# Kernel tuning notes

Hardware: AMD Instinct MI355X
Metric: run time of the kernel (lower is better)

## Reference

```python
import jax, jax.numpy as jnp
import numpy as np

N, E, G = 50000, 300000, 256
H, LAT, VOCAB = 256, 64, 100
BN_EPS = 1e-5


def _bn(x, gamma, beta):
    # BatchNorm1d in training mode: per-feature batch mean / biased var
    mu = x.mean(axis=0)
    var = x.var(axis=0)
    return gamma * (x - mu) * jax.lax.rsqrt(var + BN_EPS) + beta


def _gconv(x, edge_attr, src, dst):
    # message: softplus(x_j + e), aggregate: scatter-add to dst, update: +(1+eps)*x with eps=0
    m = jax.nn.softplus(x[src] + edge_attr)          # [E, H]
    agg = jax.ops.segment_sum(m, dst, num_segments=N)  # [N, H]
    return agg + x


def setup_inputs() -> dict:
    key = jax.random.key(0)
    ks = jax.random.split(key, 16)
    inp = {
        "node_type": jax.random.randint(ks[0], (N,), 0, VOCAB),
        "edge_type": jax.random.randint(ks[1], (E,), 0, VOCAB),
        "edge_index": jax.random.randint(ks[2], (2, E), 0, N),
        "batch": jnp.sort(jax.random.randint(ks[3], (N,), 0, G)),
        "node_emb_w": jax.random.normal(ks[4], (VOCAB, H), jnp.float32),
        "edge_emb_w": jax.random.normal(ks[5], (VOCAB, H), jnp.float32),
        "g1": jnp.ones((H,), jnp.float32), "b1": jnp.zeros((H,), jnp.float32),
        "g2": jnp.ones((H,), jnp.float32), "b2": jnp.zeros((H,), jnp.float32),
        "g3": jnp.ones((H,), jnp.float32), "b3": jnp.zeros((H,), jnp.float32),
        "go1": jnp.ones((H,), jnp.float32), "bo1": jnp.zeros((H,), jnp.float32),
        "go2": jnp.ones((H // 2,), jnp.float32), "bo2": jnp.zeros((H // 2,), jnp.float32),
        "W1": jax.random.normal(ks[6], (2 * H, H), jnp.float32) * (2 * H) ** -0.5,
        "B1": jnp.zeros((H,), jnp.float32),
        "W2": jax.random.normal(ks[7], (H, H // 2), jnp.float32) * H ** -0.5,
        "B2": jnp.zeros((H // 2,), jnp.float32),
        "W3": jax.random.normal(ks[8], (H // 2, 2 * LAT), jnp.float32) * (H // 2) ** -0.5,
        "B3": jnp.zeros((2 * LAT,), jnp.float32),
    }
    return inp


def reference(node_type, edge_type, edge_index, batch,
              node_emb_w, edge_emb_w,
              g1, b1, g2, b2, g3, b3, go1, bo1, go2, bo2,
              W1, B1, W2, B2, W3, B3):
    act = jax.nn.softplus
    src, dst = edge_index[0], edge_index[1]
    h = node_emb_w[node_type]            # [N, H]
    e = edge_emb_w[edge_type]            # [E, H]
    h = act(_bn(_gconv(h, e, src, dst), g1, b1))
    h = act(_bn(_gconv(h, e, src, dst), g2, b2))
    h = _bn(_gconv(h, e, src, dst), g3, b3)
    h_global = jax.ops.segment_sum(h, batch, num_segments=G)  # [G, H]
    feat = jnp.concatenate([h, h_global[batch]], axis=-1)     # [N, 2H]
    feat = act(_bn(feat @ W1 + B1, go1, bo1))
    feat = act(_bn(feat @ W2 + B2, go2, bo2))
    out = feat @ W3 + B3                                      # [N, 2*LAT]
    return out[:, :LAT], out[:, LAT:]
```

## Files before the change

kernel.cpp:

```cpp
#include <hip/hip_runtime.h>
#include <hip/hip_bf16.h>

namespace {

constexpr int N = 50000;
constexpr int E = 300000;
constexpr int G = 256;
constexpr int H = 256;
constexpr float EPS = 1e-5f;
constexpr int NB = (N + 255) / 256;
constexpr int POOL_S = 16;
constexpr int GBL = 256;
constexpr int NVB = N / 16;
constexpr float LOG2E = 1.4426950408889634f;
constexpr float LN2   = 0.6931471805599453f;

typedef unsigned short u16;
typedef __attribute__((ext_vector_type(8))) short bf16x8;
typedef __attribute__((ext_vector_type(4))) float f32x4;

__device__ __forceinline__ float expnabs(float z){
  float r; asm("v_exp_f32 %0, -abs(%1)" : "=v"(r) : "v"(z)); return r;
}
__device__ __forceinline__ float log2f_(float x){
  float r; asm("v_log_f32 %0, %1" : "=v"(r) : "v"(x)); return r;
}
__device__ __forceinline__ float spw(float zs){
  return fmaxf(zs, 0.f) + log2f_(1.f + expnabs(zs));
}
__device__ __forceinline__ u16 f2b(float f){
  union { float f; unsigned u; } v; v.f = f;
  unsigned r = v.u + 0x7FFF + ((v.u >> 16) & 1);
  return (u16)(r >> 16);
}
__device__ __forceinline__ float b2f(u16 u){
  union { unsigned i; float f; } v; v.i = ((unsigned)u) << 16; return v.f;
}
__device__ __forceinline__ float4 b2f4(ushort4 u){
  return make_float4(b2f(u.x), b2f(u.y), b2f(u.z), b2f(u.w));
}
__device__ __forceinline__ ushort4 f2b4(float4 v){
  ushort4 o; o.x = f2b(v.x); o.y = f2b(v.y); o.z = f2b(v.z); o.w = f2b(v.w);
  return o;
}

__device__ __forceinline__ void gl_lds16(const u16* g, u16* l){
  __builtin_amdgcn_global_load_lds(
      (const __attribute__((address_space(1))) unsigned int*)g,
      (__attribute__((address_space(3))) unsigned int*)l, 16, 0, 0);
}

__global__ void k_pre(const int* __restrict__ nt, const float* __restrict__ nemb,
                      u16* __restrict__ xb, const int* __restrict__ dst,
                      int* __restrict__ cnt,
                      const float* __restrict__ W1, const float* __restrict__ W2,
                      const float* __restrict__ W3, const float* __restrict__ eemb,
                      u16* __restrict__ Wt1, u16* __restrict__ Wt2,
                      u16* __restrict__ Wt3, float* __restrict__ eembF){
  int idx = blockIdx.x * 256 + threadIdx.x;
  if (idx < N * 64){
    int i = idx >> 6, fq = (idx & 63) << 2;
    float4 v = *(const float4*)(nemb + (size_t)nt[i] * H + fq);
    v.x *= LOG2E; v.y *= LOG2E; v.z *= LOG2E; v.w *= LOG2E;
    *(ushort4*)(xb + (size_t)i * H + fq) = f2b4(v);
    return;
  }
  int j = idx - N * 64;
  if (j < E){ atomicAdd(&cnt[dst[j]], 1); return; }
  j -= E;
  if (j < 65536){ int c = j >> 8, k = j & 255; Wt1[j] = f2b(W1[(size_t)k * 256 + c]); return; }
  j -= 65536;
  if (j < 32768){ int c = j >> 8, k = j & 255; Wt2[j] = f2b(W2[(size_t)k * 128 + c]); return; }
  j -= 32768;
  if (j < 16384){ int c = j >> 7, k = j & 127; Wt3[j] = f2b(W3[(size_t)k * 128 + c]); return; }
  j -= 16384;
  if (j < 25600) eembF[j] = eemb[j] * LOG2E;
}

__global__ void k_scan1(const int* __restrict__ cnt, int* __restrict__ bsum){
  __shared__ int s[256];
  int t = threadIdx.x;
  int i = blockIdx.x * 256 + t;
  s[t] = (i < N) ? cnt[i] : 0;
  __syncthreads();
  for (int d = 128; d > 0; d >>= 1){
    if (t < d) s[t] += s[t + d];
    __syncthreads();
  }
  if (t == 0) bsum[blockIdx.x] = s[0];
}

__global__ void k_scan2(const int* __restrict__ bsum, int* __restrict__ bbase){
  __shared__ int s[256];
  int t = threadIdx.x;
  int orig = (t < NB) ? bsum[t] : 0;
  s[t] = orig;
  __syncthreads();
  for (int d = 1; d < 256; d <<= 1){
    int v = (t >= d) ? s[t - d] : 0;
    __syncthreads();
    s[t] += v;
    __syncthreads();
  }
  bbase[t] = s[t] - orig;
}

__global__ void k_scan3(const int* __restrict__ cnt, const int* __restrict__ bbase,
                        int* __restrict__ off, int* __restrict__ cur){
  __shared__ int s[256];
  int t = threadIdx.x;
  int i = blockIdx.x * 256 + t;
  int v = (i < N) ? cnt[i] : 0;
  s[t] = v;
  __syncthreads();
  for (int d = 1; d < 256; d <<= 1){
    int u = (t >= d) ? s[t - d] : 0;
    __syncthreads();
    s[t] += u;
    __syncthreads();
  }
  int excl = bbase[blockIdx.x] + s[t] - v;
  if (i < N){ off[i] = excl; cur[i] = excl; }
  if (i == N - 1) off[N] = excl + v;
}

__global__ void k_fill(const int* __restrict__ src, const int* __restrict__ dst,
                       const int* __restrict__ et, int* __restrict__ cur,
                       int2* __restrict__ edges_s){
  int e = blockIdx.x * 256 + threadIdx.x;
  if (e >= E) return;
  int d = dst[e];
  int p = atomicAdd(&cur[d], 1);
  edges_s[p] = make_int2(src[e] << 9, et[e] << 10);
}

__device__ __forceinline__ void acc_w(float4& acc, const float4 xs, const float4 es){
  acc.x += spw(xs.x + es.x);
  acc.y += spw(xs.y + es.y);
  acc.z += spw(xs.z + es.z);
  acc.w += spw(xs.w + es.w);
}

__global__ __launch_bounds__(1024)
void k_gather(const u16* __restrict__ xb, u16* __restrict__ agg,
              const int2* __restrict__ edges_s, const int* __restrict__ off,
              const float* __restrict__ eembF,
              float* __restrict__ sums, float* __restrict__ sumsq){
  __shared__ __align__(16) float elds[25600];
  __shared__ float reds[1024][4];
  __shared__ float reds2[1024][4];
  int tid = threadIdx.x;
  int w = tid >> 6, lane = tid & 63;
  int fx = lane << 3, fe = lane << 4;
  const char* xB = (const char*)xb;
  const char* eL = (const char*)elds;

  {
    const float4* s4 = (const float4*)eembF;
    float4* d4 = (float4*)elds;
    for (int t = tid; t < 6400; t += 1024) d4[t] = s4[t];
  }
  __syncthreads();

  float4 ls = make_float4(0.f, 0.f, 0.f, 0.f);
  float4 ls2 = make_float4(0.f, 0.f, 0.f, 0.f);
  for (int vb = blockIdx.x; vb < NVB; vb += GBL){
    int i = vb * 16 + w;
    float4 acc = b2f4(*(const ushort4*)(xB + ((size_t)i << 9) + fx));
    int lo = off[i], hi = off[i + 1];
    int j = lo;
    for (; j + 4 <= hi; j += 4){
      int2 s0 = edges_s[j + 0];
      int2 s1 = edges_s[j + 1];
      int2 s2 = edges_s[j + 2];
      int2 s3 = edges_s[j + 3];
      ushort4 x0 = *(const ushort4*)(xB + s0.x + fx);
      ushort4 x1 = *(const ushort4*)(xB + s1.x + fx);
      ushort4 x2 = *(const ushort4*)(xB + s2.x + fx);
      ushort4 x3 = *(const ushort4*)(xB + s3.x + fx);
      float4 e0 = *(const float4*)(eL + s0.y + fe);
      float4 e1 = *(const float4*)(eL + s1.y + fe);
      float4 e2 = *(const float4*)(eL + s2.y + fe);
      float4 e3 = *(const float4*)(eL + s3.y + fe);
      acc_w(acc, b2f4(x0), e0);
      acc_w(acc, b2f4(x1), e1);
      acc_w(acc, b2f4(x2), e2);
      acc_w(acc, b2f4(x3), e3);
    }
    if (j + 2 <= hi){
      int2 s0 = edges_s[j + 0];
      int2 s1 = edges_s[j + 1];
      ushort4 x0 = *(const ushort4*)(xB + s0.x + fx);
      ushort4 x1 = *(const ushort4*)(xB + s1.x + fx);
      float4 e0 = *(const float4*)(eL + s0.y + fe);
      float4 e1 = *(const float4*)(eL + s1.y + fe);
      acc_w(acc, b2f4(x0), e0);
      acc_w(acc, b2f4(x1), e1);
      j += 2;
    }
    if (j < hi){
      int2 s0 = edges_s[j];
      ushort4 x0 = *(const ushort4*)(xB + s0.x + fx);
      float4 e0 = *(const float4*)(eL + s0.y + fe);
      acc_w(acc, b2f4(x0), e0);
    }
    acc.x *= LN2; acc.y *= LN2; acc.z *= LN2; acc.w *= LN2;
    ls.x += acc.x; ls.y += acc.y; ls.z += acc.z; ls.w += acc.w;
    ls2.x += acc.x * acc.x; ls2.y += acc.y * acc.y;
    ls2.z += acc.z * acc.z; ls2.w += acc.w * acc.w;
    *(ushort4*)((char*)agg + ((size_t)i << 9) + fx) = f2b4(acc);
  }
  reds[tid][0] = ls.x;  reds[tid][1] = ls.y;  reds[tid][2] = ls.z;  reds[tid][3] = ls.w;
  reds2[tid][0] = ls2.x; reds2[tid][1] = ls2.y; reds2[tid][2] = ls2.z; reds2[tid][3] = ls2.w;
  __syncthreads();
  if (tid < 256){
    int f = tid;
    float ts = 0.f, ts2 = 0.f;
    #pragma unroll
    for (int w2 = 0; w2 < 16; ++w2){
      int s = w2 * 64 + (f >> 2);
      ts += reds[s][f & 3];
      ts2 += reds2[s][f & 3];
    }
    atomicAdd(&sums[f], ts);
    atomicAdd(&sumsq[f], ts2);
  }
}

template<int ACT, int SCALED>
__global__ void k_norm(const u16* __restrict__ in, u16* __restrict__ outb,
                       const float* __restrict__ sums, const float* __restrict__ sumsq,
                       const float* __restrict__ gamma, const float* __restrict__ beta,
                       int n4, int fmask){
  int idx = blockIdx.x * 256 + threadIdx.x;
  if (idx >= n4) return;
  int base = idx << 2;
  int f = base & fmask;
  float4 s = *(const float4*)(sums + f);
  float4 q = *(const float4*)(sumsq + f);
  float4 g = *(const float4*)(gamma + f);
  float4 bt = *(const float4*)(beta + f);
  float4 v = b2f4(*(const ushort4*)(in + base));
  const float inv = 1.f / N;
  float m, var, a, c;
  m = s.x * inv; var = q.x * inv - m * m; a = g.x * rsqrtf(var + EPS); c = bt.x - m * a; v.x = a * v.x + c;
  m = s.y * inv; var = q.y * inv - m * m; a = g.y * rsqrtf(var + EPS); c = bt.y - m * a; v.y = a * v.y + c;
  m = s.z * inv; var = q.z * inv - m * m; a = g.z * rsqrtf(var + EPS); c = bt.z - m * a; v.z = a * v.z + c;
  m = s.w * inv; var = q.w * inv - m * m; a = g.w * rsqrtf(var + EPS); c = bt.w - m * a; v.w = a * v.w + c;
  if (ACT){
    v.x = spw(v.x * LOG2E); v.y = spw(v.y * LOG2E);
    v.z = spw(v.z * LOG2E); v.w = spw(v.w * LOG2E);
    if (!SCALED){ v.x *= LN2; v.y *= LN2; v.z *= LN2; v.w *= LN2; }
  }
  *(ushort4*)(outb + base) = f2b4(v);
}

__global__ void k_pool_seg(const u16* __restrict__ xb, const int* __restrict__ batch,
                           float* __restrict__ hg){
  int g = blockIdx.x, sl = blockIdx.y;
  int f = threadIdx.x;
  int lo = 0, hi = N;
  while (lo < hi){ int m = (lo + hi) >> 1; if (batch[m] < g) lo = m + 1; else hi = m; }
  int start = lo;
  lo = 0; hi = N;
  while (lo < hi){ int m = (lo + hi) >> 1; if (batch[m] < g + 1) lo = m + 1; else hi = m; }
  int end = lo;
  int len = end - start;
  int a = start + (int)((long)len * sl / POOL_S);
  int b = start + (int)((long)len * (sl + 1) / POOL_S);
  if (a >= b) return;
  float s = 0.f;
  for (int i = a; i < b; ++i) s += b2f(xb[(size_t)i * H + f]);
  atomicAdd(&hg[g * H + f], s);
}

__global__ void k_hgw(const float* __restrict__ hg, const float* __restrict__ W1,
                      const float* __restrict__ B1, float* __restrict__ hgW){
  int g = blockIdx.x, c = threadIdx.x;
  float acc = B1[c];
  for (int k = 0; k < H; ++k)
    acc += hg[g * H + k] * W1[(size_t)(H + k) * H + c];
  hgW[g * H + c] = acc;
}

template<int K, int NCOUT, int MODE, int STATS>
__global__ __launch_bounds__(256)
void k_mgemm(const u16* __restrict__ Ab, const u16* __restrict__ Wt,
             const float* __restrict__ epi, const int* __restrict__ batch,
             u16* __restrict__ outb, float* __restrict__ outf,
             float* __restrict__ sums, float* __restrict__ sumsq){
  constexpr int T = K / 64;
  __shared__ __align__(16) u16 smem[32768];
  int tid = threadIdx.x;
  int w = tid >> 6, lane = tid & 63;
  int quad = lane >> 4, l15 = lane & 15;
  int wr = w >> 1, wc = w & 1;
  int rowBase = blockIdx.x * 128 + wr * 64;
  int colTile = blockIdx.y * 128;
  const u16* Ag = Ab + (size_t)blockIdx.x * 128 * K;
  const u16* Bg = Wt + (size_t)colTile * K;

  int w6 = tid & 192;
  auto stage = [&](const u16* gbase, u16* lbuf){
    #pragma unroll
    for (int it = 0; it < 4; ++it){
      int p = it * 256 + tid;
      int row = p >> 3, slot = p & 7;
      const u16* g = gbase + (size_t)row * K + ((slot ^ (row & 7)) << 3);
      gl_lds16(g, smem + ((size_t)((lbuf - smem) + (((it * 256 + w6)) << 3))));
    }
  };

  stage(Ag, smem);
  stage(Bg, smem + 16384);

  f32x4 acc[4][4] = {};
  int xb7 = l15 & 7;
  for (int tt = 0; tt < T; ++tt){
    if (tt + 1 < T){
      int nb = (tt + 1) & 1;
      stage(Ag + (tt + 1) * 64, smem + nb * 8192);
      stage(Bg + (tt + 1) * 64, smem + 16384 + nb * 8192);
    }
    __syncthreads();
    const u16* lA = smem + (tt & 1) * 8192;
    const u16* lB = smem + 16384 + (tt & 1) * 8192;
    #pragma unroll
    for (int ks = 0; ks < 2; ++ks){
      int xs = (((ks << 2) | quad) ^ xb7) << 3;
      bf16x8 a[4], b[4];
      #pragma unroll
      for (int t = 0; t < 4; ++t)
        a[t] = *(const bf16x8*)(lA + ((wr * 64 + t * 16 + l15) << 6) + xs);
      #pragma unroll
      for (int u = 0; u < 4; ++u)
        b[u] = *(const bf16x8*)(lB + ((wc * 64 + u * 16 + l15) << 6) + xs);
      #pragma unroll
      for (int t = 0; t < 4; ++t)
        #pragma unroll
        for (int u = 0; u < 4; ++u)
          acc[t][u] = __builtin_amdgcn_mfma_f32_16x16x32_bf16(a[t], b[u], acc[t][u], 0, 0, 0);
    }
    __syncthreads();
  }

  int colBase = colTile + wc * 64;
  float ls[4] = {0.f, 0.f, 0.f, 0.f};
  float ls2[4] = {0.f, 0.f, 0.f, 0.f};
  #pragma unroll
  for (int t = 0; t < 4; ++t){
    #pragma unroll
    for (int r = 0; r < 4; ++r){
      int row = rowBase + t * 16 + quad * 4 + r;
      if (row >= N) continue;
      int g = (MODE == 0) ? batch[row] : 0;
      #pragma unroll
      for (int u = 0; u < 4; ++u){
        int n = colBase + u * 16 + l15;
        float v = acc[t][u][r];
        if (MODE == 0){
          v += epi[(size_t)g * NCOUT + n];
          outb[(size_t)row * NCOUT + n] = f2b(v);
        } else if (MODE == 1){
          v += epi[n];
          outb[(size_t)row * NCOUT + n] = f2b(v);
        } else {
          v += epi[n];
          if (n < 64) outf[(size_t)row * 64 + n] = v;
          else        outf[(size_t)N * 64 + (size_t)row * 64 + (n - 64)] = v;
        }
        if (STATS){ ls[u] += v; ls2[u] += v * v; }
      }
    }
  }
  if (STATS){
    float (*reds)[4]  = (float (*)[4])smem;
    float (*reds2)[4] = (float (*)[4])(smem + 2048);
    #pragma unroll
    for (int u = 0; u < 4; ++u){ reds[tid][u] = ls[u]; reds2[tid][u] = ls2[u]; }
    __syncthreads();
    int f = tid;
    if (f < 128){
      int fl = f & 15, fu = (f >> 4) & 3, fw = f >> 6;
      float ts = 0.f, ts2 = 0.f;
      #pragma unroll
      for (int r2 = 0; r2 < 2; ++r2)
        #pragma unroll
        for (int q = 0; q < 4; ++q){
          int s = (r2 * 2 + fw) * 64 + q * 16 + fl;
          ts += reds[s][fu]; ts2 += reds2[s][fu];
        }
      atomicAdd(&sums[colTile + f], ts);
      atomicAdd(&sumsq[colTile + f], ts2);
    }
  }
}

}

extern "C" void kernel_launch(void* const* d_in, const int* in_sizes, int n_in,
                              void* d_out, int out_size, void* d_ws, size_t ws_size,
                              hipStream_t stream){
  const int* node_type = (const int*)d_in[0];
  const int* edge_type = (const int*)d_in[1];
  const int* src       = (const int*)d_in[2];
  const int* dst       = src + E;
  const int* batch     = (const int*)d_in[3];
  const float* nemb = (const float*)d_in[4];
  const float* eemb = (const float*)d_in[5];
  const float* gs[3] = {(const float*)d_in[6], (const float*)d_in[8], (const float*)d_in[10]};
  const float* bs[3] = {(const float*)d_in[7], (const float*)d_in[9], (const float*)d_in[11]};
  const float* go1 = (const float*)d_in[12]; const float* bo1 = (const float*)d_in[13];
  const float* go2 = (const float*)d_in[14]; const float* bo2 = (const float*)d_in[15];
  const float* W1 = (const float*)d_in[16]; const float* B1 = (const float*)d_in[17];
  const float* W2 = (const float*)d_in[18]; const float* B2 = (const float*)d_in[19];
  const float* W3 = (const float*)d_in[20]; const float* B3 = (const float*)d_in[21];
  float* outf = (float*)d_out;

  char* p = (char*)d_ws;
  int*   cnt    = (int*)p;              p += (size_t)N * 4;
  float* hg     = (float*)p;            p += (size_t)G * H * 4;
  float* statsA = (float*)p;            p += 5 * 512 * 4;
  size_t zeroBytes = (size_t)p - (size_t)d_ws;
  float* hgW    = (float*)p;            p += (size_t)G * H * 4;
  int*   off    = (int*)p;              p += (size_t)(N + 1) * 4;
  int*   cur    = (int*)p;              p += (size_t)N * 4;
  int*   bsum   = (int*)p;              p += 256 * 4;
  int*   bbase  = (int*)p;              p += 256 * 4;
  int2*  edges_s= (int2*)p;             p += (size_t)E * 8;
  u16*   xb     = (u16*)p;              p += (size_t)N * H * 2;
  u16*   agg    = (u16*)p;              p += (size_t)N * H * 2;
  u16*   xf     = (u16*)p;              p += (size_t)N * 128 * 2;
  u16*   Wt1    = (u16*)p;              p += 65536 * 2;
  u16*   Wt2    = (u16*)p;              p += 32768 * 2;
  u16*   Wt3    = (u16*)p;              p += 16384 * 2;
  float* eembF  = (float*)p;            p += 25600 * 4;
  float* sumsL[5], *sumsqL[5];
  for (int k = 0; k < 5; ++k){ sumsL[k] = statsA + k * 512; sumsqL[k] = statsA + k * 512 + 256; }

  hipMemsetAsync(d_ws, 0, zeroBytes, stream);

  const int preItems = N * 64 + E + 65536 + 32768 + 16384 + 25600;
  k_pre<<<(preItems + 255) / 256, 256, 0, stream>>>(
      node_type, nemb, xb, dst, cnt, W1, W2, W3, eemb, Wt1, Wt2, Wt3, eembF);
  k_scan1<<<NB, 256, 0, stream>>>(cnt, bsum);
  k_scan2<<<1, 256, 0, stream>>>(bsum, bbase);
  k_scan3<<<NB, 256, 0, stream>>>(cnt, bbase, off, cur);
  k_fill<<<(E + 255) / 256, 256, 0, stream>>>(src, dst, edge_type, cur, edges_s);

  for (int l = 0; l < 3; ++l){
    k_gather<<<GBL, 1024, 0, stream>>>(xb, agg, edges_s, off, eembF, sumsL[l], sumsqL[l]);
    if (l < 2)
      k_norm<1, 1><<<(N * 64 + 255) / 256, 256, 0, stream>>>(
          agg, xb, sumsL[l], sumsqL[l], gs[l], bs[l], N * 64, 255);
    else
      k_norm<0, 0><<<(N * 64 + 255) / 256, 256, 0, stream>>>(
          agg, xb, sumsL[l], sumsqL[l], gs[l], bs[l], N * 64, 255);
  }

  {
    dim3 pg(G, POOL_S);
    k_pool_seg<<<pg, H, 0, stream>>>(xb, batch, hg);
  }
  k_hgw<<<G, H, 0, stream>>>(hg, W1, B1, hgW);

  const int RB = (N + 127) / 128;

  k_mgemm<256, 256, 0, 1><<<dim3(RB, 2), 256, 0, stream>>>(
      xb, Wt1, hgW, batch, agg, nullptr, sumsL[3], sumsqL[3]);
  k_norm<1, 0><<<(N * 64 + 255) / 256, 256, 0, stream>>>(
      agg, xb, sumsL[3], sumsqL[3], go1, bo1, N * 64, 255);

  k_mgemm<256, 128, 1, 1><<<dim3(RB, 1), 256, 0, stream>>>(
      xb, Wt2, B2, nullptr, xf, nullptr, sumsL[4], sumsqL[4]);
  k_norm<1, 0><<<(N * 32 + 255) / 256, 256, 0, stream>>>(
      xf, xb, sumsL[4], sumsqL[4], go2, bo2, N * 32, 127);

  k_mgemm<128, 128, 2, 0><<<dim3(RB, 1), 256, 0, stream>>>(
      xb, Wt3, B3, nullptr, nullptr, outf, nullptr, nullptr);
}
```

Before: 455.0 us.

## Store edge embedding table in LDS as fp16 and double gather grid

The edge-embedding table kept in LDS by the gather kernel is switched from fp32 to fp16, halving its shared-memory footprint. The large per-thread reduction arrays are replaced by LDS atomics into 256-entry accumulators, and the grid is doubled from 256 to 512 blocks. Together these cut LDS use per block so more 1024-thread blocks can be resident per CU, raising occupancy for the latency-bound gather. The cost is fp16 rounding of the scaled edge embeddings and contention on the LDS atomics.

Result: slower. 498.8 us (+9.6%).

```diff
diff --git a/kernel.cpp b/kernel.cpp
--- a/kernel.cpp
+++ b/kernel.cpp
@@ -1,5 +1,6 @@
 #include <hip/hip_runtime.h>
 #include <hip/hip_bf16.h>
+#include <hip/hip_fp16.h>
 
 namespace {
 
@@ -10,7 +11,7 @@
 constexpr float EPS = 1e-5f;
 constexpr int NB = (N + 255) / 256;
 constexpr int POOL_S = 16;
-constexpr int GBL = 256;
+constexpr int GBL = 512;
 constexpr int NVB = N / 16;
 constexpr float LOG2E = 1.4426950408889634f;
 constexpr float LN2   = 0.6931471805599453f;
@@ -18,6 +19,7 @@
 typedef unsigned short u16;
 typedef __attribute__((ext_vector_type(8))) short bf16x8;
 typedef __attribute__((ext_vector_type(4))) float f32x4;
+typedef _Float16 f16x4 __attribute__((ext_vector_type(4)));
 
 __device__ __forceinline__ float expnabs(float z){
   float r; asm("v_exp_f32 %0, -abs(%1)" : "=v"(r) : "v"(z)); return r;
@@ -56,7 +58,7 @@
                       const float* __restrict__ W1, const float* __restrict__ W2,
                       const float* __restrict__ W3, const float* __restrict__ eemb,
                       u16* __restrict__ Wt1, u16* __restrict__ Wt2,
-                      u16* __restrict__ Wt3, float* __restrict__ eembF){
+                      u16* __restrict__ Wt3, u16* __restrict__ eembH){
   int idx = blockIdx.x * 256 + threadIdx.x;
   if (idx < N * 64){
     int i = idx >> 6, fq = (idx & 63) << 2;
@@ -74,7 +76,10 @@
   j -= 32768;
   if (j < 16384){ int c = j >> 7, k = j & 127; Wt3[j] = f2b(W3[(size_t)k * 128 + c]); return; }
   j -= 16384;
-  if (j < 25600) eembF[j] = eemb[j] * LOG2E;
+  if (j < 25600){
+    _Float16 h = (_Float16)(eemb[j] * LOG2E);
+    eembH[j] = *(const u16*)&h;
+  }
 }
 
 __global__ void k_scan1(const int* __restrict__ cnt, int* __restrict__ bsum){
@@ -131,7 +136,7 @@
   if (e >= E) return;
   int d = dst[e];
   int p = atomicAdd(&cur[d], 1);
-  edges_s[p] = make_int2(src[e] << 9, et[e] << 10);
+  edges_s[p] = make_int2(src[e] << 9, et[e] << 9);
 }
 
 __device__ __forceinline__ void acc_w(float4& acc, const float4 xs, const float4 es){
@@ -140,25 +145,30 @@
   acc.z += spw(xs.z + es.z);
   acc.w += spw(xs.w + es.w);
 }
+__device__ __forceinline__ float4 h2f4(f16x4 h){
+  return make_float4((float)h[0], (float)h[1], (float)h[2], (float)h[3]);
+}
 
 __global__ __launch_bounds__(1024)
 void k_gather(const u16* __restrict__ xb, u16* __restrict__ agg,
               const int2* __restrict__ edges_s, const int* __restrict__ off,
-              const float* __restrict__ eembF,
+              const u16* __restrict__ eembH,
               float* __restrict__ sums, float* __restrict__ sumsq){
-  __shared__ __align__(16) float elds[25600];
-  __shared__ float reds[1024][4];
-  __shared__ float reds2[1024][4];
+  __shared__ __align__(16) u16 elds[25600];
+  __shared__ float ssum[256];
+  __shared__ float ssum2[256];
   int tid = threadIdx.x;
   int w = tid >> 6, lane = tid & 63;
-  int fx = lane << 3, fe = lane << 4;
+  int fx = lane << 3;
+  int fe = lane << 3;
   const char* xB = (const char*)xb;
   const char* eL = (const char*)elds;
 
   {
-    const float4* s4 = (const float4*)eembF;
-    float4* d4 = (float4*)elds;
-    for (int t = tid; t < 6400; t += 1024) d4[t] = s4[t];
+    const uint4* s4 = (const uint4*)eembH;
+    uint4* d4 = (uint4*)elds;
+    for (int t = tid; t < 3200; t += 1024) d4[t] = s4[t];
+    if (tid < 256){ ssum[tid] = 0.f; ssum2[tid] = 0.f; }
   }
   __syncthreads();
 
@@ -178,31 +188,31 @@
       ushort4 x1 = *(const ushort4*)(xB + s1.x + fx);
       ushort4 x2 = *(const ushort4*)(xB + s2.x + fx);
       ushort4 x3 = *(const ushort4*)(xB + s3.x + fx);
-      float4 e0 = *(const float4*)(eL + s0.y + fe);
-      float4 e1 = *(const float4*)(eL + s1.y + fe);
-      float4 e2 = *(const float4*)(eL + s2.y + fe);
-      float4 e3 = *(const float4*)(eL + s3.y + fe);
-      acc_w(acc, b2f4(x0), e0);
-      acc_w(acc, b2f4(x1), e1);
-      acc_w(acc, b2f4(x2), e2);
-      acc_w(acc, b2f4(x3), e3);
+      f16x4 e0 = *(const f16x4*)(eL + s0.y + fe);
+      f16x4 e1 = *(const f16x4*)(eL + s1.y + fe);
+      f16x4 e2 = *(const f16x4*)(eL + s2.y + fe);
+      f16x4 e3 = *(const f16x4*)(eL + s3.y + fe);
+      acc_w(acc, b2f4(x0), h2f4(e0));
+      acc_w(acc, b2f4(x1), h2f4(e1));
+      acc_w(acc, b2f4(x2), h2f4(e2));
+      acc_w(acc, b2f4(x3), h2f4(e3));
     }
     if (j + 2 <= hi){
       int2 s0 = edges_s[j + 0];
       int2 s1 = edges_s[j + 1];
       ushort4 x0 = *(const ushort4*)(xB + s0.x + fx);
       ushort4 x1 = *(const ushort4*)(xB + s1.x + fx);
-      float4 e0 = *(const float4*)(eL + s0.y + fe);
-      float4 e1 = *(const float4*)(eL + s1.y + fe);
-      acc_w(acc, b2f4(x0), e0);
-      acc_w(acc, b2f4(x1), e1);
+      f16x4 e0 = *(const f16x4*)(eL + s0.y + fe);
+      f16x4 e1 = *(const f16x4*)(eL + s1.y + fe);
+      acc_w(acc, b2f4(x0), h2f4(e0));
+      acc_w(acc, b2f4(x1), h2f4(e1));
       j += 2;
     }
     if (j < hi){
       int2 s0 = edges_s[j];
       ushort4 x0 = *(const ushort4*)(xB + s0.x + fx);
-      float4 e0 = *(const float4*)(eL + s0.y + fe);
-      acc_w(acc, b2f4(x0), e0);
+      f16x4 e0 = *(const f16x4*)(eL + s0.y + fe);
+      acc_w(acc, b2f4(x0), h2f4(e0));
     }
     acc.x *= LN2; acc.y *= LN2; acc.z *= LN2; acc.w *= LN2;
     ls.x += acc.x; ls.y += acc.y; ls.z += acc.z; ls.w += acc.w;
@@ -210,20 +220,15 @@
     ls2.z += acc.z * acc.z; ls2.w += acc.w * acc.w;
     *(ushort4*)((char*)agg + ((size_t)i << 9) + fx) = f2b4(acc);
   }
-  reds[tid][0] = ls.x;  reds[tid][1] = ls.y;  reds[tid][2] = ls.z;  reds[tid][3] = ls.w;
-  reds2[tid][0] = ls2.x; reds2[tid][1] = ls2.y; reds2[tid][2] = ls2.z; reds2[tid][3] = ls2.w;
+  int fb = lane << 2;
+  atomicAdd(&ssum[fb + 0], ls.x);  atomicAdd(&ssum2[fb + 0], ls2.x);
+  atomicAdd(&ssum[fb + 1], ls.y);  atomicAdd(&ssum2[fb + 1], ls2.y);
+  atomicAdd(&ssum[fb + 2], ls.z);  atomicAdd(&ssum2[fb + 2], ls2.z);
+  atomicAdd(&ssum[fb + 3], ls.w);  atomicAdd(&ssum2[fb + 3], ls2.w);
   __syncthreads();
   if (tid < 256){
-    int f = tid;
-    float ts = 0.f, ts2 = 0.f;
-    #pragma unroll
-    for (int w2 = 0; w2 < 16; ++w2){
-      int s = w2 * 64 + (f >> 2);
-      ts += reds[s][f & 3];
-      ts2 += reds2[s][f & 3];
-    }
-    atomicAdd(&sums[f], ts);
-    atomicAdd(&sumsq[f], ts2);
+    atomicAdd(&sums[tid], ssum[tid]);
+    atomicAdd(&sumsq[tid], ssum2[tid]);
   }
 }
 
@@ -434,7 +439,7 @@
   u16*   Wt1    = (u16*)p;              p += 65536 * 2;
   u16*   Wt2    = (u16*)p;              p += 32768 * 2;
   u16*   Wt3    = (u16*)p;              p += 16384 * 2;
-  float* eembF  = (float*)p;            p += 25600 * 4;
+  u16*   eembH  = (u16*)p;              p += 25600 * 4;
   float* sumsL[5], *sumsqL[5];
   for (int k = 0; k < 5; ++k){ sumsL[k] = statsA + k * 512; sumsqL[k] = statsA + k * 512 + 256; }
 
@@ -442,14 +447,14 @@
 
   const int preItems = N * 64 + E + 65536 + 32768 + 16384 + 25600;
   k_pre<<<(preItems + 255) / 256, 256, 0, stream>>>(
-      node_type, nemb, xb, dst, cnt, W1, W2, W3, eemb, Wt1, Wt2, Wt3, eembF);
+      node_type, nemb, xb, dst, cnt, W1, W2, W3, eemb, Wt1, Wt2, Wt3, eembH);
   k_scan1<<<NB, 256, 0, stream>>>(cnt, bsum);
   k_scan2<<<1, 256, 0, stream>>>(bsum, bbase);
   k_scan3<<<NB, 256, 0, stream>>>(cnt, bbase, off, cur);
   k_fill<<<(E + 255) / 256, 256, 0, stream>>>(src, dst, edge_type, cur, edges_s);
 
   for (int l = 0; l < 3; ++l){
-    k_gather<<<GBL, 1024, 0, stream>>>(xb, agg, edges_s, off, eembF, sumsL[l], sumsqL[l]);
+    k_gather<<<GBL, 1024, 0, stream>>>(xb, agg, edges_s, off, eembH, sumsL[l], sumsqL[l]);
     if (l < 2)
       k_norm<1, 1><<<(N * 64 + 255) / 256, 256, 0, stream>>>(
           agg, xb, sumsL[l], sumsqL[l], gs[l], bs[l], N * 64, 255);
```

## Fuse previous layer's batchnorm and softplus into the gather kernel

Applied to the files above, without the earlier changes.

The gather kernel gains an APPLY template mode that rebuilds the previous layer's BN scale and shift from its accumulated sums and applies BN plus softplus on the fly to every gathered neighbour and self row. This removes the two standalone normalize passes between conv layers, and the agg and xb buffers now ping-pong between layers. The cost is recomputing the affine transform and an extra softplus for every edge read instead of once per node, which adds transcendental work to the gather's inner loop.

New measurement: 468.8 us. +3.0%, slower.

```diff
diff --git a/kernel.cpp b/kernel.cpp
--- a/kernel.cpp
+++ b/kernel.cpp
@@ -141,18 +141,21 @@
   acc.w += spw(xs.w + es.w);
 }
 
+template<int APPLY>
 __global__ __launch_bounds__(1024)
-void k_gather(const u16* __restrict__ xb, u16* __restrict__ agg,
+void k_gather(const u16* __restrict__ xin, u16* __restrict__ agg,
               const int2* __restrict__ edges_s, const int* __restrict__ off,
               const float* __restrict__ eembF,
-              float* __restrict__ sums, float* __restrict__ sumsq){
+              float* __restrict__ sums, float* __restrict__ sumsq,
+              const float* __restrict__ pg, const float* __restrict__ pb,
+              const float* __restrict__ psums, const float* __restrict__ psumsq){
   __shared__ __align__(16) float elds[25600];
   __shared__ float reds[1024][4];
   __shared__ float reds2[1024][4];
   int tid = threadIdx.x;
   int w = tid >> 6, lane = tid & 63;
   int fx = lane << 3, fe = lane << 4;
-  const char* xB = (const char*)xb;
+  const char* xB = (const char*)xin;
   const char* eL = (const char*)elds;
 
   {
@@ -162,11 +165,36 @@
   }
   __syncthreads();
 
+  float4 A = make_float4(0.f,0.f,0.f,0.f), C = make_float4(0.f,0.f,0.f,0.f);
+  if (APPLY){
+    int f = lane << 2;
+    float4 s = *(const float4*)(psums + f);
+    float4 q = *(const float4*)(psumsq + f);
+    float4 g = *(const float4*)(pg + f);
+    float4 bt = *(const float4*)(pb + f);
+    const float inv = 1.f / N;
+    float m, var, a;
+    m = s.x*inv; var = q.x*inv - m*m; a = g.x*rsqrtf(var+EPS); A.x = a*LOG2E; C.x = (bt.x - m*a)*LOG2E;
+    m = s.y*inv; var = q.y*inv - m*m; a = g.y*rsqrtf(var+EPS); A.y = a*LOG2E; C.y = (bt.y - m*a)*LOG2E;
+    m = s.z*inv; var = q.z*inv - m*m; a = g.z*rsqrtf(var+EPS); A.z = a*LOG2E; C.z = (bt.z - m*a)*LOG2E;
+    m = s.w*inv; var = q.w*inv - m*m; a = g.w*rsqrtf(var+EPS); A.w = a*LOG2E; C.w = (bt.w - m*a)*LOG2E;
+  }
+  auto xform = [&](ushort4 u) -> float4 {
+    float4 v = b2f4(u);
+    if (APPLY){
+      v.x = spw(A.x * v.x + C.x);
+      v.y = spw(A.y * v.y + C.y);
+      v.z = spw(A.z * v.z + C.z);
+      v.w = spw(A.w * v.w + C.w);
+    }
+    return v;
+  };
+
   float4 ls = make_float4(0.f, 0.f, 0.f, 0.f);
   float4 ls2 = make_float4(0.f, 0.f, 0.f, 0.f);
   for (int vb = blockIdx.x; vb < NVB; vb += GBL){
     int i = vb * 16 + w;
-    float4 acc = b2f4(*(const ushort4*)(xB + ((size_t)i << 9) + fx));
+    float4 acc = xform(*(const ushort4*)(xB + ((size_t)i << 9) + fx));
     int lo = off[i], hi = off[i + 1];
     int j = lo;
     for (; j + 4 <= hi; j += 4){
@@ -182,10 +210,10 @@
       float4 e1 = *(const float4*)(eL + s1.y + fe);
       float4 e2 = *(const float4*)(eL + s2.y + fe);
       float4 e3 = *(const float4*)(eL + s3.y + fe);
-      acc_w(acc, b2f4(x0), e0);
-      acc_w(acc, b2f4(x1), e1);
-      acc_w(acc, b2f4(x2), e2);
-      acc_w(acc, b2f4(x3), e3);
+      acc_w(acc, xform(x0), e0);
+      acc_w(acc, xform(x1), e1);
+      acc_w(acc, xform(x2), e2);
+      acc_w(acc, xform(x3), e3);
     }
     if (j + 2 <= hi){
       int2 s0 = edges_s[j + 0];
@@ -194,15 +222,15 @@
       ushort4 x1 = *(const ushort4*)(xB + s1.x + fx);
       float4 e0 = *(const float4*)(eL + s0.y + fe);
       float4 e1 = *(const float4*)(eL + s1.y + fe);
-      acc_w(acc, b2f4(x0), e0);
-      acc_w(acc, b2f4(x1), e1);
+      acc_w(acc, xform(x0), e0);
+      acc_w(acc, xform(x1), e1);
       j += 2;
     }
     if (j < hi){
       int2 s0 = edges_s[j];
       ushort4 x0 = *(const ushort4*)(xB + s0.x + fx);
       float4 e0 = *(const float4*)(eL + s0.y + fe);
-      acc_w(acc, b2f4(x0), e0);
+      acc_w(acc, xform(x0), e0);
     }
     acc.x *= LN2; acc.y *= LN2; acc.z *= LN2; acc.w *= LN2;
     ls.x += acc.x; ls.y += acc.y; ls.z += acc.z; ls.w += acc.w;
@@ -448,15 +476,17 @@
   k_scan3<<<NB, 256, 0, stream>>>(cnt, bbase, off, cur);
   k_fill<<<(E + 255) / 256, 256, 0, stream>>>(src, dst, edge_type, cur, edges_s);
 
-  for (int l = 0; l < 3; ++l){
-    k_gather<<<GBL, 1024, 0, stream>>>(xb, agg, edges_s, off, eembF, sumsL[l], sumsqL[l]);
-    if (l < 2)
-      k_norm<1, 1><<<(N * 64 + 255) / 256, 256, 0, stream>>>(
-          agg, xb, sumsL[l], sumsqL[l], gs[l], bs[l], N * 64, 255);
-    else
-      k_norm<0, 0><<<(N * 64 + 255) / 256, 256, 0, stream>>>(
-          agg, xb, sumsL[l], sumsqL[l], gs[l], bs[l], N * 64, 255);
-  }
+  k_gather<0><<<GBL, 1024, 0, stream>>>(
+      xb, agg, edges_s, off, eembF, sumsL[0], sumsqL[0],
+      nullptr, nullptr, nullptr, nullptr);
+  k_gather<1><<<GBL, 1024, 0, stream>>>(
+      agg, xb, edges_s, off, eembF, sumsL[1], sumsqL[1],
+      gs[0], bs[0], sumsL[0], sumsqL[0]);
+  k_gather<1><<<GBL, 1024, 0, stream>>>(
+      xb, agg, edges_s, off, eembF, sumsL[2], sumsqL[2],
+      gs[1], bs[1], sumsL[1], sumsqL[1]);
+  k_norm<0, 0><<<(N * 64 + 255) / 256, 256, 0, stream>>>(
+      agg, xb, sumsL[2], sumsqL[2], gs[2], bs[2], N * 64, 255);
 
   {
     dim3 pg(G, POOL_S);
```

## Fuse three GNN layers with batchnorm into one cooperative persistent kernel

Applied to the files above, without the earlier changes.

Replaces the six per-layer gather and norm launches with a single cooperative kernel that loops over the three layers and uses grid-wide syncs between the aggregation, statistics and normalization phases. The edge embedding table is loaded into shared memory once instead of once per layer, and five kernel launches are removed. In exchange, grid.sync barriers are added, the norm phase now runs on only 256 blocks of 1024 threads, and co-residency of all blocks is required for the cooperative launch.

Measured after the change: 668.1 us. 46.9% more time.

```diff
diff --git a/kernel.cpp b/kernel.cpp
--- a/kernel.cpp
+++ b/kernel.cpp
@@ -1,5 +1,8 @@
 #include <hip/hip_runtime.h>
 #include <hip/hip_bf16.h>
+#include <hip/hip_cooperative_groups.h>
+
+namespace cg = cooperative_groups;
 
 namespace {
 
@@ -142,17 +145,19 @@
 }
 
 __global__ __launch_bounds__(1024)
-void k_gather(const u16* __restrict__ xb, u16* __restrict__ agg,
-              const int2* __restrict__ edges_s, const int* __restrict__ off,
-              const float* __restrict__ eembF,
-              float* __restrict__ sums, float* __restrict__ sumsq){
+void k_gnn(u16* __restrict__ xb, u16* __restrict__ agg,
+           const int2* __restrict__ edges_s, const int* __restrict__ off,
+           const float* __restrict__ eembF, float* __restrict__ statsA,
+           const float* __restrict__ g0, const float* __restrict__ b0,
+           const float* __restrict__ g1, const float* __restrict__ b1,
+           const float* __restrict__ g2, const float* __restrict__ b2){
+  cg::grid_group grid = cg::this_grid();
   __shared__ __align__(16) float elds[25600];
   __shared__ float reds[1024][4];
   __shared__ float reds2[1024][4];
   int tid = threadIdx.x;
   int w = tid >> 6, lane = tid & 63;
   int fx = lane << 3, fe = lane << 4;
-  const char* xB = (const char*)xb;
   const char* eL = (const char*)elds;
 
   {
@@ -162,68 +167,99 @@
   }
   __syncthreads();
 
-  float4 ls = make_float4(0.f, 0.f, 0.f, 0.f);
-  float4 ls2 = make_float4(0.f, 0.f, 0.f, 0.f);
-  for (int vb = blockIdx.x; vb < NVB; vb += GBL){
-    int i = vb * 16 + w;
-    float4 acc = b2f4(*(const ushort4*)(xB + ((size_t)i << 9) + fx));
-    int lo = off[i], hi = off[i + 1];
-    int j = lo;
-    for (; j + 4 <= hi; j += 4){
-      int2 s0 = edges_s[j + 0];
-      int2 s1 = edges_s[j + 1];
-      int2 s2 = edges_s[j + 2];
-      int2 s3 = edges_s[j + 3];
-      ushort4 x0 = *(const ushort4*)(xB + s0.x + fx);
-      ushort4 x1 = *(const ushort4*)(xB + s1.x + fx);
-      ushort4 x2 = *(const ushort4*)(xB + s2.x + fx);
-      ushort4 x3 = *(const ushort4*)(xB + s3.x + fx);
-      float4 e0 = *(const float4*)(eL + s0.y + fe);
-      float4 e1 = *(const float4*)(eL + s1.y + fe);
-      float4 e2 = *(const float4*)(eL + s2.y + fe);
-      float4 e3 = *(const float4*)(eL + s3.y + fe);
-      acc_w(acc, b2f4(x0), e0);
-      acc_w(acc, b2f4(x1), e1);
-      acc_w(acc, b2f4(x2), e2);
-      acc_w(acc, b2f4(x3), e3);
-    }
-    if (j + 2 <= hi){
-      int2 s0 = edges_s[j + 0];
-      int2 s1 = edges_s[j + 1];
-      ushort4 x0 = *(const ushort4*)(xB + s0.x + fx);
-      ushort4 x1 = *(const ushort4*)(xB + s1.x + fx);
-      float4 e0 = *(const float4*)(eL + s0.y + fe);
-      float4 e1 = *(const float4*)(eL + s1.y + fe);
-      acc_w(acc, b2f4(x0), e0);
-      acc_w(acc, b2f4(x1), e1);
-      j += 2;
-    }
-    if (j < hi){
-      int2 s0 = edges_s[j];
-      ushort4 x0 = *(const ushort4*)(xB + s0.x + fx);
-      float4 e0 = *(const float4*)(eL + s0.y + fe);
-      acc_w(acc, b2f4(x0), e0);
-    }
-    acc.x *= LN2; acc.y *= LN2; acc.z *= LN2; acc.w *= LN2;
-    ls.x += acc.x; ls.y += acc.y; ls.z += acc.z; ls.w += acc.w;
-    ls2.x += acc.x * acc.x; ls2.y += acc.y * acc.y;
-    ls2.z += acc.z * acc.z; ls2.w += acc.w * acc.w;
-    *(ushort4*)((char*)agg + ((size_t)i << 9) + fx) = f2b4(acc);
-  }
-  reds[tid][0] = ls.x;  reds[tid][1] = ls.y;  reds[tid][2] = ls.z;  reds[tid][3] = ls.w;
-  reds2[tid][0] = ls2.x; reds2[tid][1] = ls2.y; reds2[tid][2] = ls2.z; reds2[tid][3] = ls2.w;
-  __syncthreads();
-  if (tid < 256){
-    int f = tid;
-    float ts = 0.f, ts2 = 0.f;
-    #pragma unroll
-    for (int w2 = 0; w2 < 16; ++w2){
-      int s = w2 * 64 + (f >> 2);
-      ts += reds[s][f & 3];
-      ts2 += reds2[s][f & 3];
-    }
-    atomicAdd(&sums[f], ts);
-    atomicAdd(&sumsq[f], ts2);
+  const float inv = 1.f / N;
+  for (int l = 0; l < 3; ++l){
+    float* sums  = statsA + l * 512;
+    float* sumsq = sums + 256;
+    const char* xB = (const char*)xb;
+
+    float4 ls = make_float4(0.f, 0.f, 0.f, 0.f);
+    float4 ls2 = make_float4(0.f, 0.f, 0.f, 0.f);
+    for (int vb = blockIdx.x; vb < NVB; vb += GBL){
+      int i = vb * 16 + w;
+      float4 acc = b2f4(*(const ushort4*)(xB + ((size_t)i << 9) + fx));
+      int lo = off[i], hi = off[i + 1];
+      int j = lo;
+      for (; j + 4 <= hi; j += 4){
+        int2 s0 = edges_s[j + 0];
+        int2 s1 = edges_s[j + 1];
+        int2 s2 = edges_s[j + 2];
+        int2 s3 = edges_s[j + 3];
+        ushort4 x0 = *(const ushort4*)(xB + s0.x + fx);
+        ushort4 x1 = *(const ushort4*)(xB + s1.x + fx);
+        ushort4 x2 = *(const ushort4*)(xB + s2.x + fx);
+        ushort4 x3 = *(const ushort4*)(xB + s3.x + fx);
+        float4 e0 = *(const float4*)(eL + s0.y + fe);
+        float4 e1 = *(const float4*)(eL + s1.y + fe);
+        float4 e2 = *(const float4*)(eL + s2.y + fe);
+        float4 e3 = *(const float4*)(eL + s3.y + fe);
+        acc_w(acc, b2f4(x0), e0);
+        acc_w(acc, b2f4(x1), e1);
+        acc_w(acc, b2f4(x2), e2);
+        acc_w(acc, b2f4(x3), e3);
+      }
+      if (j + 2 <= hi){
+        int2 s0 = edges_s[j + 0];
+        int2 s1 = edges_s[j + 1];
+        ushort4 x0 = *(const ushort4*)(xB + s0.x + fx);
+        ushort4 x1 = *(const ushort4*)(xB + s1.x + fx);
+        float4 e0 = *(const float4*)(eL + s0.y + fe);
+        float4 e1 = *(const float4*)(eL + s1.y + fe);
+        acc_w(acc, b2f4(x0), e0);
+        acc_w(acc, b2f4(x1), e1);
+        j += 2;
+      }
+      if (j < hi){
+        int2 s0 = edges_s[j];
+        ushort4 x0 = *(const ushort4*)(xB + s0.x + fx);
+        float4 e0 = *(const float4*)(eL + s0.y + fe);
+        acc_w(acc, b2f4(x0), e0);
+      }
+      acc.x *= LN2; acc.y *= LN2; acc.z *= LN2; acc.w *= LN2;
+      ls.x += acc.x; ls.y += acc.y; ls.z += acc.z; ls.w += acc.w;
+      ls2.x += acc.x * acc.x; ls2.y += acc.y * acc.y;
+      ls2.z += acc.z * acc.z; ls2.w += acc.w * acc.w;
+      *(ushort4*)((char*)agg + ((size_t)i << 9) + fx) = f2b4(acc);
+    }
+    reds[tid][0] = ls.x;  reds[tid][1] = ls.y;  reds[tid][2] = ls.z;  reds[tid][3] = ls.w;
+    reds2[tid][0] = ls2.x; reds2[tid][1] = ls2.y; reds2[tid][2] = ls2.z; reds2[tid][3] = ls2.w;
+    __syncthreads();
+    if (tid < 256){
+      int f = tid;
+      float ts = 0.f, ts2 = 0.f;
+      #pragma unroll
+      for (int w2 = 0; w2 < 16; ++w2){
+        int s = w2 * 64 + (f >> 2);
+        ts += reds[s][f & 3];
+        ts2 += reds2[s][f & 3];
+      }
+      atomicAdd(&sums[f], ts);
+      atomicAdd(&sumsq[f], ts2);
+    }
+    grid.sync();
+
+    const float* gamma = (l == 0) ? g0 : (l == 1) ? g1 : g2;
+    const float* beta  = (l == 0) ? b0 : (l == 1) ? b1 : b2;
+    for (int idx = blockIdx.x * 1024 + tid; idx < N * 64; idx += GBL * 1024){
+      int base = idx << 2;
+      int f = base & 255;
+      float4 s = *(const float4*)(sums + f);
+      float4 q = *(const float4*)(sumsq + f);
+      float4 g = *(const float4*)(gamma + f);
+      float4 bt = *(const float4*)(beta + f);
+      float4 v = b2f4(*(const ushort4*)(agg + base));
+      float m, var, a, c;
+      m = s.x * inv; var = q.x * inv - m * m; a = g.x * rsqrtf(var + EPS); c = bt.x - m * a; v.x = a * v.x + c;
+      m = s.y * inv; var = q.y * inv - m * m; a = g.y * rsqrtf(var + EPS); c = bt.y - m * a; v.y = a * v.y + c;
+      m = s.z * inv; var = q.z * inv - m * m; a = g.z * rsqrtf(var + EPS); c = bt.z - m * a; v.z = a * v.z + c;
+      m = s.w * inv; var = q.w * inv - m * m; a = g.w * rsqrtf(var + EPS); c = bt.w - m * a; v.w = a * v.w + c;
+      if (l < 2){
+        v.x = spw(v.x * LOG2E); v.y = spw(v.y * LOG2E);
+        v.z = spw(v.z * LOG2E); v.w = spw(v.w * LOG2E);
+      }
+      *(ushort4*)(xb + base) = f2b4(v);
+    }
+    grid.sync();
   }
 }
 
@@ -448,14 +484,12 @@
   k_scan3<<<NB, 256, 0, stream>>>(cnt, bbase, off, cur);
   k_fill<<<(E + 255) / 256, 256, 0, stream>>>(src, dst, edge_type, cur, edges_s);
 
-  for (int l = 0; l < 3; ++l){
-    k_gather<<<GBL, 1024, 0, stream>>>(xb, agg, edges_s, off, eembF, sumsL[l], sumsqL[l]);
-    if (l < 2)
-      k_norm<1, 1><<<(N * 64 + 255) / 256, 256, 0, stream>>>(
-          agg, xb, sumsL[l], sumsqL[l], gs[l], bs[l], N * 64, 255);
-    else
-      k_norm<0, 0><<<(N * 64 + 255) / 256, 256, 0, stream>>>(
-          agg, xb, sumsL[l], sumsqL[l], gs[l], bs[l], N * 64, 255);
+  {
+    const float *g0 = gs[0], *b0 = bs[0], *g1 = gs[1], *b1 = bs[1], *g2 = gs[2], *b2 = bs[2];
+    void* kargs[] = {(void*)&xb, (void*)&agg, (void*)&edges_s, (void*)&off,
+                     (void*)&eembF, (void*)&statsA,
+                     (void*)&g0, (void*)&b0, (void*)&g1, (void*)&b1, (void*)&g2, (void*)&b2};
+    hipLaunchCooperativeKernel((void*)k_gnn, dim3(GBL), dim3(1024), kargs, 0, stream);
   }
 
   {
```
